# Performance work log

Hardware: AMD Instinct MI355X
Metric: run time of the kernel (lower is better)

Reference implementation:

```python
import jax, jax.numpy as jnp
import numpy as np

HIDDEN = 2048
NUM_Q_HEADS = 32
NUM_KV_HEADS = 8
HEAD_DIM = HIDDEN // NUM_Q_HEADS  # 64
GROUPS = NUM_Q_HEADS // NUM_KV_HEADS  # 4
MAX_WAVELENGTH = 10000.0
B, S = 2, 1024
NEG_INF = -1e9  # keras Softmax masking constant


def apply_rope(x, start_index=0, max_wavelength=MAX_WAVELENGTH):
    # x: [b, s, h, d]; keras_hub RotaryEmbedding (split-half / Llama style)
    d = x.shape[-1]
    s = x.shape[1]
    freq_range = jnp.arange(0, d, 2, dtype=jnp.float32)
    inverse_freq = 1.0 / (max_wavelength ** (freq_range / d))  # [d/2]
    positions = jnp.arange(s, dtype=jnp.float32) + start_index
    freq = positions[:, None] * inverse_freq[None, :]  # [s, d/2]
    emb = jnp.concatenate([freq, freq], axis=-1)[None, :, None, :]  # [1,s,1,d]
    cos = jnp.cos(emb).astype(x.dtype)
    sin = jnp.sin(emb).astype(x.dtype)
    x1, x2 = jnp.split(x, 2, axis=-1)
    half_rot = jnp.concatenate([-x2, x1], axis=-1)
    return x * cos + half_rot * sin


def setup_inputs() -> dict:
    key = jax.random.key(0)
    k1, k2, k3, k4, k5 = jax.random.split(key, 5)
    hidden_states = jax.random.normal(k1, (B, S, HIDDEN), dtype=jnp.float32)
    # causal mask, broadcast over batch
    attention_mask = jnp.broadcast_to(
        jnp.tril(jnp.ones((S, S), dtype=bool))[None], (B, S, S)
    )
    scale = 1.0 / np.sqrt(HIDDEN)
    Wq = jax.random.normal(k2, (HIDDEN, NUM_Q_HEADS * HEAD_DIM), dtype=jnp.float32) * scale
    Wk = jax.random.normal(k3, (HIDDEN, NUM_KV_HEADS * HEAD_DIM), dtype=jnp.float32) * scale
    Wv = jax.random.normal(k4, (HIDDEN, NUM_KV_HEADS * HEAD_DIM), dtype=jnp.float32) * scale
    Wo = jax.random.normal(k5, (NUM_Q_HEADS * HEAD_DIM, HIDDEN), dtype=jnp.float32) * scale
    return {"hidden_states": hidden_states, "attention_mask": attention_mask,
            "Wq": Wq, "Wk": Wk, "Wv": Wv, "Wo": Wo}


def reference(hidden_states, attention_mask, Wq, Wk, Wv, Wo):
    b, s, _ = hidden_states.shape
    q = (hidden_states @ Wq).reshape(b, s, NUM_Q_HEADS, HEAD_DIM)
    k = (hidden_states @ Wk).reshape(b, s, NUM_KV_HEADS, HEAD_DIM)
    v = (hidden_states @ Wv).reshape(b, s, NUM_KV_HEADS, HEAD_DIM)
    q = apply_rope(q)
    k = apply_rope(k)
    # GQA: repeat kv heads to match query heads (ops.repeat on axis 2)
    k = jnp.repeat(k, GROUPS, axis=2)
    v = jnp.repeat(v, GROUPS, axis=2)
    inv_norm = 1.0 / np.sqrt(HEAD_DIM)
    scores = jnp.einsum("bquh,bkuh->buqk", q, k) * inv_norm  # [b, h, q, k]
    scores = scores.astype(jnp.float32)
    scores = jnp.where(attention_mask[:, None, :, :], scores, NEG_INF)
    probs = jax.nn.softmax(scores, axis=-1).astype(hidden_states.dtype)
    attn = jnp.einsum("buqk,bkuh->bquh", probs, v)  # [b, q, h, hd]
    attn = attn.reshape(b, s, HIDDEN)
    return attn @ Wo
```

## Files before the change

### kernel.cpp

```cpp
#include <hip/hip_runtime.h>
#include <hip/hip_bf16.h>
#include <math.h>

#define S_LEN 1024
#define BATCH 2
#define HIDDEN 2048
#define NQH 32
#define NKVH 8
#define HD 64
#define LDQKV 3072
#define M_ROWS (BATCH * S_LEN)

typedef __attribute__((ext_vector_type(8))) short bf16x8;
typedef __attribute__((ext_vector_type(4))) float f32x4;

typedef unsigned int uint32_g __attribute__((address_space(1)));
typedef unsigned int uint32_l __attribute__((address_space(3)));

static __device__ __forceinline__ void load_lds16(const void* g, void* l) {
    __builtin_amdgcn_global_load_lds((const uint32_g*)g, (uint32_l*)l, 16, 0, 0);
}

static __device__ __forceinline__ short f2bf(float f) {
    union { __hip_bfloat16 h; short s; } cv;
    cv.h = __float2bfloat16(f);
    return cv.s;
}

__global__ __launch_bounds__(256) void conv_all_kernel(
    const float* __restrict__ X,
    const float* __restrict__ Wq, const float* __restrict__ Wk,
    const float* __restrict__ Wv, const float* __restrict__ Wo,
    short* __restrict__ Xb, short* __restrict__ Wqkvt, short* __restrict__ Wot,
    float2* __restrict__ cs2)
{
    __shared__ short Ts[64][68];
    const int tid = threadIdx.x;

    if (blockIdx.z == 4) {
        int flat = blockIdx.y * 32 + blockIdx.x;
        size_t base = (size_t)flat * 4096 + (size_t)tid * 16;
        #pragma unroll
        for (int rep = 0; rep < 2; ++rep) {
            size_t i = base + rep * 8;
            float4 a = *reinterpret_cast<const float4*>(X + i);
            float4 b = *reinterpret_cast<const float4*>(X + i + 4);
            union { bf16x8 v; short s[8]; } t;
            t.s[0] = f2bf(a.x); t.s[1] = f2bf(a.y); t.s[2] = f2bf(a.z); t.s[3] = f2bf(a.w);
            t.s[4] = f2bf(b.x); t.s[5] = f2bf(b.y); t.s[6] = f2bf(b.z); t.s[7] = f2bf(b.w);
            *reinterpret_cast<bf16x8*>(Xb + i) = t.v;
        }
        if (flat < 128) {
            int g = flat * 256 + tid;
            int s = g >> 5, i = g & 31;
            float inv_freq = 1.0f / powf(10000.0f, (float)i / 32.0f);
            float freq = (float)s * inv_freq;
            double sn, cs;
            sincos((double)freq, &sn, &cs);
            cs2[g] = make_float2((float)cs, (float)sn);
        }
        return;
    }

    const float* src; short* dst; int N;
    switch (blockIdx.z) {
        case 0: src = Wq; dst = Wqkvt;                         N = 2048; break;
        case 1: src = Wk; dst = Wqkvt + (size_t)2048 * 2048;   N = 512;  break;
        case 2: src = Wv; dst = Wqkvt + (size_t)2560 * 2048;   N = 512;  break;
        default: src = Wo; dst = Wot;                          N = 2048; break;
    }
    const int n0 = blockIdx.x * 64, k0 = blockIdx.y * 64;
    if (n0 >= N) return;

    #pragma unroll
    for (int rep = 0; rep < 4; ++rep) {
        int idx = rep * 256 + tid;
        int row = idx >> 4, c4 = (idx & 15) * 4;
        float4 v = *reinterpret_cast<const float4*>(
            src + (size_t)(k0 + row) * N + n0 + c4);
        ushort4 u;
        u.x = (unsigned short)f2bf(v.x); u.y = (unsigned short)f2bf(v.y);
        u.z = (unsigned short)f2bf(v.z); u.w = (unsigned short)f2bf(v.w);
        *reinterpret_cast<ushort4*>(&Ts[row][c4]) = u;
    }
    __syncthreads();
    #pragma unroll
    for (int rep = 0; rep < 2; ++rep) {
        int idx = rep * 256 + tid;
        int n = idx >> 3, kc = (idx & 7) * 8;
        union { bf16x8 v; short s[8]; } t;
        #pragma unroll
        for (int j = 0; j < 8; ++j) t.s[j] = Ts[kc + j][n];
        *reinterpret_cast<bf16x8*>(dst + (size_t)(n0 + n) * 2048 + k0 + kc) = t.v;
    }
}

template <bool ROPE_BF16>
__global__ __launch_bounds__(256) void gemm_bf16_kernel(
    const short* __restrict__ A, const short* __restrict__ Bt,
    float* __restrict__ C, short* __restrict__ Cb,
    short* __restrict__ vt_g,
    const float2* __restrict__ cs2, int K, int ldc)
{
    const int n0 = blockIdx.x * 64, m0 = blockIdx.y * 128;
    const int tid = threadIdx.x;
    const int w = tid >> 6, lane = tid & 63;
    const int m15 = lane & 15, q4 = lane >> 4;

    __shared__ short SL[2][128 * 64 + 64 * 64];

    f32x4 acc[2][4];
    #pragma unroll
    for (int i = 0; i < 2; ++i)
        #pragma unroll
        for (int j = 0; j < 4; ++j) acc[i][j] = (f32x4){0.f, 0.f, 0.f, 0.f};

    const int srow = lane >> 3;
    const int pchunk = lane & 7;

#define GSTAGE(bf_, k0_) do {                                                 \
    short (*As_)[64] = (short(*)[64])SL[bf_];                                 \
    short (*Bs_)[64] = (short(*)[64])(SL[bf_] + 128 * 64);                    \
    _Pragma("unroll")                                                         \
    for (int r = 0; r < 4; ++r) {                                             \
        int row = (w * 4 + r) * 8 + srow;                         \
        int lchunk = pchunk ^ (row & 7);                                      \
        load_lds16(A + (size_t)(m0 + row) * K + (k0_) + lchunk * 8,           \
                   &As_[(w * 4 + r) * 8][0]);                                 \
    }                                                                         \
    _Pragma("unroll")                                                         \
    for (int r = 0; r < 2; ++r) {                                             \
        int row = (w * 2 + r) * 8 + srow;                          \
        int lchunk = pchunk ^ (row & 7);                                      \
        load_lds16(Bt + (size_t)(n0 + row) * K + (k0_) + lchunk * 8,          \
                   &Bs_[(w * 2 + r) * 8][0]);                                 \
    }                                                                         \
} while (0)

    GSTAGE(0, 0);
    __syncthreads();

    const int nkt = K >> 6;
    for (int kt = 0; kt < nkt; ++kt) {
        const int bf = kt & 1;
        if (kt + 1 < nkt) GSTAGE(bf ^ 1, (kt + 1) * 64);

        short (*As)[64] = (short(*)[64])SL[bf];
        short (*Bs)[64] = (short(*)[64])(SL[bf] + 128 * 64);
        #pragma unroll
        for (int ch = 0; ch < 2; ++ch) {
            bf16x8 af[2], bff[4];
            #pragma unroll
            for (int mt = 0; mt < 2; ++mt) {
                int row = w * 32 + mt * 16 + m15;
                af[mt] = *reinterpret_cast<const bf16x8*>(
                    &As[row][(((ch * 4 + q4) ^ (row & 7))) * 8]);
            }
            #pragma unroll
            for (int nt = 0; nt < 4; ++nt) {
                int row = nt * 16 + m15;
                bff[nt] = *reinterpret_cast<const bf16x8*>(
                    &Bs[row][(((ch * 4 + q4) ^ (row & 7))) * 8]);
            }
            #pragma unroll
            for (int mt = 0; mt < 2; ++mt)
                #pragma unroll
                for (int nt = 0; nt < 4; ++nt)
                    acc[mt][nt] = __builtin_amdgcn_mfma_f32_16x16x32_bf16(
                        af[mt], bff[nt], acc[mt][nt], 0, 0, 0);
        }
        __syncthreads();
    }
#undef GSTAGE

    if (!ROPE_BF16) {
        #pragma unroll
        for (int mt = 0; mt < 2; ++mt)
            #pragma unroll
            for (int nt = 0; nt < 4; ++nt)
                #pragma unroll
                for (int reg = 0; reg < 4; ++reg)
                    C[(size_t)(m0 + w * 32 + mt * 16 + q4 * 4 + reg) * ldc
                      + n0 + nt * 16 + m15] = acc[mt][nt][reg];
    } else if (n0 < 2560) {
        #pragma unroll
        for (int mt = 0; mt < 2; ++mt) {
            #pragma unroll
            for (int reg = 0; reg < 4; ++reg) {
                int row = m0 + w * 32 + mt * 16 + q4 * 4 + reg;
                int s = row & (S_LEN - 1);
                float2 t0 = cs2[s * 32 + m15];
                float2 t1 = cs2[s * 32 + 16 + m15];
                float a0 = acc[mt][0][reg], a1 = acc[mt][1][reg];
                float a2 = acc[mt][2][reg], a3 = acc[mt][3][reg];
                size_t base = (size_t)row * ldc + n0 + m15;
                Cb[base +  0] = f2bf(a0 * t0.x - a2 * t0.y);
                Cb[base + 16] = f2bf(a1 * t1.x - a3 * t1.y);
                Cb[base + 32] = f2bf(a2 * t0.x + a0 * t0.y);
                Cb[base + 48] = f2bf(a3 * t1.x + a1 * t1.y);
            }
        }
    } else {
        __syncthreads();
        short (*VT)[136] = (short(*)[136])SL[0];
        #pragma unroll
        for (int mt = 0; mt < 2; ++mt) {
            #pragma unroll
            for (int nt = 0; nt < 4; ++nt) {
                ushort4 u;
                u.x = (unsigned short)f2bf(acc[mt][nt][0]);
                u.y = (unsigned short)f2bf(acc[mt][nt][1]);
                u.z = (unsigned short)f2bf(acc[mt][nt][2]);
                u.w = (unsigned short)f2bf(acc[mt][nt][3]);
                *reinterpret_cast<ushort4*>(
                    &VT[nt * 16 + m15][w * 32 + mt * 16 + q4 * 4]) = u;
            }
        }
        __syncthreads();
        const int kvh = (n0 - 2560) >> 6;
        const int b = m0 >> 10, k0loc = m0 & (S_LEN - 1);
        const int dim = tid >> 2, kc = (tid & 3) * 32;
        short* dst = vt_g + (size_t)((b * 8 + kvh) * 64 + dim) * S_LEN + k0loc + kc;
        #pragma unroll
        for (int u = 0; u < 4; ++u)
            *reinterpret_cast<bf16x8*>(dst + u * 8) =
                *reinterpret_cast<const bf16x8*>(&VT[dim][kc + u * 8]);
    }
}

__global__ __launch_bounds__(512, 4) void attn_kernel(
    const short* __restrict__ qkvb, const short* __restrict__ vt_g,
    short* __restrict__ attn_b)
{
    const int i  = blockIdx.x;
    const int h  = blockIdx.y;
    const int b  = blockIdx.z;
    const int qtA = i;
    const int qtB = 15 - i;
    const int tid = threadIdx.x;
    const int w = tid >> 6, lane = tid & 63;
    const int kvh = h >> 2;
    const int m15 = lane & 15, q4 = lane >> 4;

    __shared__ short Ks[2][64][64];
    __shared__ short Vt[2][64][64];

    const int qt_w = (w < 4) ? qtB : qtA;
    const int rowbase = qt_w * 64 + (w & 3) * 16;

    const bf16x8 qf0 = *reinterpret_cast<const bf16x8*>(
        qkvb + (size_t)(b * S_LEN + rowbase + m15) * LDQKV + h * HD + q4 * 8);
    const bf16x8 qf1 = *reinterpret_cast<const bf16x8*>(
        qkvb + (size_t)(b * S_LEN + rowbase + m15) * LDQKV + h * HD + 32 + q4 * 8);

    f32x4 o4[4];
    #pragma unroll
    for (int k = 0; k < 4; ++k) o4[k] = (f32x4){0.f, 0.f, 0.f, 0.f};
    float lsum = 0.f;

    const int r8 = lane >> 3, p8 = lane & 7;
    const int lch = (p8 ^ r8) * 8;
    const short* kbase = qkvb + (size_t)(b * S_LEN) * LDQKV + 2048 + kvh * HD;
    const short* vbase = vt_g + (size_t)(b * 8 + kvh) * 64 * S_LEN;

#define STAGE(bf_, t) do {                                                    \
    int row_ = w * 8 + r8;                                                    \
    load_lds16(kbase + (size_t)((t) * 64 + row_) * LDQKV + lch,               \
               &Ks[bf_][w * 8][0]);                                           \
    load_lds16(vbase + (size_t)row_ * S_LEN + (t) * 64 + lch,                 \
               &Vt[bf_][w * 8][0]);                                           \
} while (0)

#define COMPUTE(bf_, t) do {                                                  \
    const int xr_ = m15 & 7;                                                  \
    float p_[4][4];                                                           \
    _Pragma("unroll")                                                         \
    for (int nt = 0; nt < 4; ++nt) {                                          \
        f32x4 acc = (f32x4){0.f, 0.f, 0.f, 0.f};                              \
        bf16x8 kf0 = *reinterpret_cast<const bf16x8*>(                        \
            &Ks[bf_][nt * 16 + m15][(q4 ^ xr_) * 8]);                         \
        bf16x8 kf1 = *reinterpret_cast<const bf16x8*>(                        \
            &Ks[bf_][nt * 16 + m15][((4 + q4) ^ xr_) * 8]);                   \
        acc = __builtin_amdgcn_mfma_f32_16x16x32_bf16(kf0, qf0, acc, 0, 0, 0);\
        acc = __builtin_amdgcn_mfma_f32_16x16x32_bf16(kf1, qf1, acc, 0, 0, 0);\
        _Pragma("unroll")                                                     \
        for (int reg = 0; reg < 4; ++reg)                                     \
            p_[nt][reg] = exp2f(fminf(acc[reg] * 0.180336880f, 80.f));        \
    }                                                                         \
    if ((t) * 64 + 63 > rowbase) {            \
        const int rowg_ = rowbase + m15;                                      \
        _Pragma("unroll")                                                     \
        for (int nt = 0; nt < 4; ++nt)                                        \
            _Pragma("unroll")                                                 \
            for (int reg = 0; reg < 4; ++reg)                                 \
                if ((t) * 64 + nt * 16 + q4 * 4 + reg > rowg_)                \
                    p_[nt][reg] = 0.f;                                        \
    }                                                                         \
    _Pragma("unroll")                                                         \
    for (int nt = 0; nt < 4; ++nt)                                            \
        _Pragma("unroll")                                                     \
        for (int reg = 0; reg < 4; ++reg) lsum += p_[nt][reg];                \
    unsigned lo_[4], hi_[4];                                                  \
    _Pragma("unroll")                                                         \
    for (int nt = 0; nt < 4; ++nt) {                                          \
        lo_[nt] = (unsigned)(unsigned short)f2bf(p_[nt][0])                   \
                | ((unsigned)(unsigned short)f2bf(p_[nt][1]) << 16);          \
        hi_[nt] = (unsigned)(unsigned short)f2bf(p_[nt][2])                   \
                | ((unsigned)(unsigned short)f2bf(p_[nt][3]) << 16);          \
    }                                                                         \
    const int La_ = ((q4 & 1) * 2) * 16 + m15;                                \
    const int Lb_ = La_ + 16;                                                 \
    const int hiH_ = q4 >> 1;                                                 \
    bf16x8 pf_[2];                                                            \
    _Pragma("unroll")                                                         \
    for (int ch = 0; ch < 2; ++ch) {                                          \
        int a0 = __shfl((int)lo_[ch * 2],     La_, 64);                       \
        int a1 = __shfl((int)hi_[ch * 2],     La_, 64);                       \
        int a2 = __shfl((int)lo_[ch * 2],     Lb_, 64);                       \
        int a3 = __shfl((int)hi_[ch * 2],     Lb_, 64);                       \
        int b0 = __shfl((int)lo_[ch * 2 + 1], La_, 64);                       \
        int b1 = __shfl((int)hi_[ch * 2 + 1], La_, 64);                       \
        int b2 = __shfl((int)lo_[ch * 2 + 1], Lb_, 64);                       \
        int b3 = __shfl((int)hi_[ch * 2 + 1], Lb_, 64);                       \
        union { int ii[4]; bf16x8 v; } u_;                                    \
        u_.ii[0] = hiH_ ? b0 : a0;                                            \
        u_.ii[1] = hiH_ ? b1 : a1;                                            \
        u_.ii[2] = hiH_ ? b2 : a2;                                            \
        u_.ii[3] = hiH_ ? b3 : a3;                                            \
        pf_[ch] = u_.v;                                                       \
    }                                                                         \
    _Pragma("unroll")                                                         \
    for (int nt2 = 0; nt2 < 4; ++nt2) {                                       \
        bf16x8 vf0 = *reinterpret_cast<const bf16x8*>(                        \
            &Vt[bf_][nt2 * 16 + m15][(q4 ^ xr_) * 8]);                        \
        bf16x8 vf1 = *reinterpret_cast<const bf16x8*>(                        \
            &Vt[bf_][nt2 * 16 + m15][((4 + q4) ^ xr_) * 8]);                  \
        o4[nt2] = __builtin_amdgcn_mfma_f32_16x16x32_bf16(                    \
            pf_[0], vf0, o4[nt2], 0, 0, 0);                                   \
        o4[nt2] = __builtin_amdgcn_mfma_f32_16x16x32_bf16(                    \
            pf_[1], vf1, o4[nt2], 0, 0, 0);                                   \
    }                                                                         \
} while (0)

    STAGE(0, 0);
    __syncthreads();

    for (int t = 0; t <= qtB; ++t) {
        const int bf = t & 1;
        if (t < qtB) STAGE(bf ^ 1, t + 1);
        if (t <= qt_w) COMPUTE(bf, t);
        __syncthreads();
    }

#undef STAGE
#undef COMPUTE

    float l = lsum;
    l += __shfl_xor(l, 16, 64);
    l += __shfl_xor(l, 32, 64);
    float invl = 1.0f / l;
    float invl4[4];
    #pragma unroll
    for (int reg = 0; reg < 4; ++reg)
        invl4[reg] = __shfl(invl, q4 * 4 + reg, 64);

    #pragma unroll
    for (int nt2 = 0; nt2 < 4; ++nt2)
        #pragma unroll
        for (int reg = 0; reg < 4; ++reg)
            attn_b[(size_t)(b * S_LEN + rowbase + q4 * 4 + reg) * HIDDEN
                   + h * HD + nt2 * 16 + m15] = f2bf(o4[nt2][reg] * invl4[reg]);
}

extern "C" void kernel_launch(void* const* d_in, const int* in_sizes, int n_in,
                              void* d_out, int out_size, void* d_ws, size_t ws_size,
                              hipStream_t stream) {
    const float* X  = (const float*)d_in[0];
    const float* Wq = (const float*)d_in[2];
    const float* Wk = (const float*)d_in[3];
    const float* Wv = (const float*)d_in[4];
    const float* Wo = (const float*)d_in[5];
    float* out = (float*)d_out;

    short*  qkvb  = (short*)d_ws;
    short*  Xb    = qkvb + (size_t)M_ROWS * LDQKV;
    short*  Wqkvt = Xb + (size_t)HIDDEN * HIDDEN;
    short*  Wot   = Wqkvt + (size_t)LDQKV * HIDDEN;
    short*  vt_g  = Wot + (size_t)HIDDEN * HIDDEN;
    float2* cs2   = (float2*)(vt_g + (size_t)16 * 64 * S_LEN);
    short*  attn_b = Xb;

    conv_all_kernel<<<dim3(32, 32, 5), dim3(256), 0, stream>>>(
        X, Wq, Wk, Wv, Wo, Xb, Wqkvt, Wot, cs2);

    gemm_bf16_kernel<true><<<dim3(48, 16), dim3(256), 0, stream>>>(
        Xb, Wqkvt, nullptr, qkvb, vt_g, cs2, 2048, LDQKV);
    attn_kernel<<<dim3(8, 32, 2), dim3(512), 0, stream>>>(qkvb, vt_g, attn_b);
    gemm_bf16_kernel<false><<<dim3(32, 16), dim3(256), 0, stream>>>(
        attn_b, Wot, out, nullptr, nullptr, nullptr, 2048, HIDDEN);
}
```

Measured before the change: 194.7 us.

## Load K and V fragments directly from global memory, dropping LDS staging

Removes the double-buffered LDS staging of K and V tiles, along with the per-tile block-wide barriers, in the attention kernel. Each wave now reads its K and V MFMA fragments straight from global memory (relying on L1/L2 caching) and loops only up to its own causal tile count. This removes the synchronisation and LDS traffic, and lets each wave run independently of the others. The cost is that the eight waves fetch the same K/V data redundantly from cache, and the global loads have higher latency with no prefetch overlap.

```diff
diff --git a/kernel.cpp b/kernel.cpp
--- a/kernel.cpp
+++ b/kernel.cpp
@@ -242,9 +242,6 @@
     const int kvh = h >> 2;
     const int m15 = lane & 15, q4 = lane >> 4;
 
-    __shared__ short Ks[2][64][64];
-    __shared__ short Vt[2][64][64];
-
     const int qt_w = (w < 4) ? qtB : qtA;
     const int rowbase = qt_w * 64 + (w & 3) * 16;
 
@@ -258,29 +255,18 @@
     for (int k = 0; k < 4; ++k) o4[k] = (f32x4){0.f, 0.f, 0.f, 0.f};
     float lsum = 0.f;
 
-    const int r8 = lane >> 3, p8 = lane & 7;
-    const int lch = (p8 ^ r8) * 8;
     const short* kbase = qkvb + (size_t)(b * S_LEN) * LDQKV + 2048 + kvh * HD;
     const short* vbase = vt_g + (size_t)(b * 8 + kvh) * 64 * S_LEN;
 
-#define STAGE(bf_, t) do {                                                    \
-    int row_ = w * 8 + r8;                                                    \
-    load_lds16(kbase + (size_t)((t) * 64 + row_) * LDQKV + lch,               \
-               &Ks[bf_][w * 8][0]);                                           \
-    load_lds16(vbase + (size_t)row_ * S_LEN + (t) * 64 + lch,                 \
-               &Vt[bf_][w * 8][0]);                                           \
-} while (0)
-
-#define COMPUTE(bf_, t) do {                                                  \
-    const int xr_ = m15 & 7;                                                  \
+#define COMPUTE(t) do {                                                       \
     float p_[4][4];                                                           \
     _Pragma("unroll")                                                         \
     for (int nt = 0; nt < 4; ++nt) {                                          \
         f32x4 acc = (f32x4){0.f, 0.f, 0.f, 0.f};                              \
-        bf16x8 kf0 = *reinterpret_cast<const bf16x8*>(                        \
-            &Ks[bf_][nt * 16 + m15][(q4 ^ xr_) * 8]);                         \
-        bf16x8 kf1 = *reinterpret_cast<const bf16x8*>(                        \
-            &Ks[bf_][nt * 16 + m15][((4 + q4) ^ xr_) * 8]);                   \
+        const short* krow_ = kbase                                            \
+            + (size_t)((t) * 64 + nt * 16 + m15) * LDQKV;                     \
+        bf16x8 kf0 = *reinterpret_cast<const bf16x8*>(krow_ + q4 * 8);        \
+        bf16x8 kf1 = *reinterpret_cast<const bf16x8*>(krow_ + 32 + q4 * 8);   \
         acc = __builtin_amdgcn_mfma_f32_16x16x32_bf16(kf0, qf0, acc, 0, 0, 0);\
         acc = __builtin_amdgcn_mfma_f32_16x16x32_bf16(kf1, qf1, acc, 0, 0, 0);\
         _Pragma("unroll")                                                     \
@@ -331,10 +317,10 @@
     }                                                                         \
     _Pragma("unroll")                                                         \
     for (int nt2 = 0; nt2 < 4; ++nt2) {                                       \
-        bf16x8 vf0 = *reinterpret_cast<const bf16x8*>(                        \
-            &Vt[bf_][nt2 * 16 + m15][(q4 ^ xr_) * 8]);                        \
-        bf16x8 vf1 = *reinterpret_cast<const bf16x8*>(                        \
-            &Vt[bf_][nt2 * 16 + m15][((4 + q4) ^ xr_) * 8]);                  \
+        const short* vrow_ = vbase                                            \
+            + (size_t)(nt2 * 16 + m15) * S_LEN + (t) * 64;                    \
+        bf16x8 vf0 = *reinterpret_cast<const bf16x8*>(vrow_ + q4 * 8);        \
+        bf16x8 vf1 = *reinterpret_cast<const bf16x8*>(vrow_ + 32 + q4 * 8);   \
         o4[nt2] = __builtin_amdgcn_mfma_f32_16x16x32_bf16(                    \
             pf_[0], vf0, o4[nt2], 0, 0, 0);                                   \
         o4[nt2] = __builtin_amdgcn_mfma_f32_16x16x32_bf16(                    \
@@ -342,17 +328,10 @@
     }                                                                         \
 } while (0)
 
-    STAGE(0, 0);
-    __syncthreads();
-
-    for (int t = 0; t <= qtB; ++t) {
-        const int bf = t & 1;
-        if (t < qtB) STAGE(bf ^ 1, t + 1);
-        if (t <= qt_w) COMPUTE(bf, t);
-        __syncthreads();
-    }
-
-#undef STAGE
+    for (int t = 0; t <= qt_w; ++t) {
+        COMPUTE(t);
+    }
+
 #undef COMPUTE
 
     float l = lsum;
```

After: 232.4 us. +19.4%, slower.

## Balance causal attention waves by splitting long query tile KV range across idle waves

Applied to the files above, without the earlier changes.

The attention kernel pairs query tiles i and 15-i per block. Previously the waves on the short tile sat idle while the waves on the long tile walked up to 16 KV tiles. Now the loop runs 9 iterations. Once the short tile is finished, its waves process the later KV tiles of the long tile into separate accumulators, and the partial outputs and row sums are merged through LDS at the end. This shortens the critical path per block. In exchange it doubles the LDS buffers, stages two KV tiles per iteration, and adds a merge step with an extra barrier.

```diff
diff --git a/kernel.cpp b/kernel.cpp
--- a/kernel.cpp
+++ b/kernel.cpp
@@ -241,54 +241,62 @@
     const int w = tid >> 6, lane = tid & 63;
     const int kvh = h >> 2;
     const int m15 = lane & 15, q4 = lane >> 4;
-
-    __shared__ short Ks[2][64][64];
-    __shared__ short Vt[2][64][64];
-
-    const int qt_w = (w < 4) ? qtB : qtA;
-    const int rowbase = qt_w * 64 + (w & 3) * 16;
-
-    const bf16x8 qf0 = *reinterpret_cast<const bf16x8*>(
-        qkvb + (size_t)(b * S_LEN + rowbase + m15) * LDQKV + h * HD + q4 * 8);
-    const bf16x8 qf1 = *reinterpret_cast<const bf16x8*>(
-        qkvb + (size_t)(b * S_LEN + rowbase + m15) * LDQKV + h * HD + 32 + q4 * 8);
-
-    f32x4 o4[4];
+    const int wq = w & 3;
+
+    __shared__ short Ks[2][2][64][64];
+    __shared__ short Vt[2][2][64][64];
+
+    const int rowbaseB = qtB * 64 + wq * 16;
+    const int rowbaseA = qtA * 64 + wq * 16;
+
+    const bf16x8 qfB0 = *reinterpret_cast<const bf16x8*>(
+        qkvb + (size_t)(b * S_LEN + rowbaseB + m15) * LDQKV + h * HD + q4 * 8);
+    const bf16x8 qfB1 = *reinterpret_cast<const bf16x8*>(
+        qkvb + (size_t)(b * S_LEN + rowbaseB + m15) * LDQKV + h * HD + 32 + q4 * 8);
+    const bf16x8 qfA0 = *reinterpret_cast<const bf16x8*>(
+        qkvb + (size_t)(b * S_LEN + rowbaseA + m15) * LDQKV + h * HD + q4 * 8);
+    const bf16x8 qfA1 = *reinterpret_cast<const bf16x8*>(
+        qkvb + (size_t)(b * S_LEN + rowbaseA + m15) * LDQKV + h * HD + 32 + q4 * 8);
+
+    f32x4 oB[4], oA[4];
     #pragma unroll
-    for (int k = 0; k < 4; ++k) o4[k] = (f32x4){0.f, 0.f, 0.f, 0.f};
-    float lsum = 0.f;
+    for (int k = 0; k < 4; ++k) {
+        oB[k] = (f32x4){0.f, 0.f, 0.f, 0.f};
+        oA[k] = (f32x4){0.f, 0.f, 0.f, 0.f};
+    }
+    float lB = 0.f, lA = 0.f;
 
     const int r8 = lane >> 3, p8 = lane & 7;
     const int lch = (p8 ^ r8) * 8;
     const short* kbase = qkvb + (size_t)(b * S_LEN) * LDQKV + 2048 + kvh * HD;
     const short* vbase = vt_g + (size_t)(b * 8 + kvh) * 64 * S_LEN;
 
-#define STAGE(bf_, t) do {                                                    \
+#define STAGE(bf_, sl_, tk) do {                                              \
     int row_ = w * 8 + r8;                                                    \
-    load_lds16(kbase + (size_t)((t) * 64 + row_) * LDQKV + lch,               \
-               &Ks[bf_][w * 8][0]);                                           \
-    load_lds16(vbase + (size_t)row_ * S_LEN + (t) * 64 + lch,                 \
-               &Vt[bf_][w * 8][0]);                                           \
+    load_lds16(kbase + (size_t)((tk) * 64 + row_) * LDQKV + lch,              \
+               &Ks[bf_][sl_][w * 8][0]);                                      \
+    load_lds16(vbase + (size_t)row_ * S_LEN + (tk) * 64 + lch,                \
+               &Vt[bf_][sl_][w * 8][0]);                                      \
 } while (0)
 
-#define COMPUTE(bf_, t) do {                                                  \
+#define COMPUTE(bf_, sl_, t, rb_, o_, ls_, qa_, qb_) do {                     \
     const int xr_ = m15 & 7;                                                  \
     float p_[4][4];                                                           \
     _Pragma("unroll")                                                         \
     for (int nt = 0; nt < 4; ++nt) {                                          \
         f32x4 acc = (f32x4){0.f, 0.f, 0.f, 0.f};                              \
         bf16x8 kf0 = *reinterpret_cast<const bf16x8*>(                        \
-            &Ks[bf_][nt * 16 + m15][(q4 ^ xr_) * 8]);                         \
+            &Ks[bf_][sl_][nt * 16 + m15][(q4 ^ xr_) * 8]);                    \
         bf16x8 kf1 = *reinterpret_cast<const bf16x8*>(                        \
-            &Ks[bf_][nt * 16 + m15][((4 + q4) ^ xr_) * 8]);                   \
-        acc = __builtin_amdgcn_mfma_f32_16x16x32_bf16(kf0, qf0, acc, 0, 0, 0);\
-        acc = __builtin_amdgcn_mfma_f32_16x16x32_bf16(kf1, qf1, acc, 0, 0, 0);\
+            &Ks[bf_][sl_][nt * 16 + m15][((4 + q4) ^ xr_) * 8]);              \
+        acc = __builtin_amdgcn_mfma_f32_16x16x32_bf16(kf0, qa_, acc, 0, 0, 0);\
+        acc = __builtin_amdgcn_mfma_f32_16x16x32_bf16(kf1, qb_, acc, 0, 0, 0);\
         _Pragma("unroll")                                                     \
         for (int reg = 0; reg < 4; ++reg)                                     \
             p_[nt][reg] = exp2f(fminf(acc[reg] * 0.180336880f, 80.f));        \
     }                                                                         \
-    if ((t) * 64 + 63 > rowbase) {            \
-        const int rowg_ = rowbase + m15;                                      \
+    if ((t) * 64 + 63 > (rb_)) {              \
+        const int rowg_ = (rb_) + m15;                                        \
         _Pragma("unroll")                                                     \
         for (int nt = 0; nt < 4; ++nt)                                        \
             _Pragma("unroll")                                                 \
@@ -299,7 +307,7 @@
     _Pragma("unroll")                                                         \
     for (int nt = 0; nt < 4; ++nt)                                            \
         _Pragma("unroll")                                                     \
-        for (int reg = 0; reg < 4; ++reg) lsum += p_[nt][reg];                \
+        for (int reg = 0; reg < 4; ++reg) (ls_) += p_[nt][reg];               \
     unsigned lo_[4], hi_[4];                                                  \
     _Pragma("unroll")                                                         \
     for (int nt = 0; nt < 4; ++nt) {                                          \
@@ -332,44 +340,93 @@
     _Pragma("unroll")                                                         \
     for (int nt2 = 0; nt2 < 4; ++nt2) {                                       \
         bf16x8 vf0 = *reinterpret_cast<const bf16x8*>(                        \
-            &Vt[bf_][nt2 * 16 + m15][(q4 ^ xr_) * 8]);                        \
+            &Vt[bf_][sl_][nt2 * 16 + m15][(q4 ^ xr_) * 8]);                   \
         bf16x8 vf1 = *reinterpret_cast<const bf16x8*>(                        \
-            &Vt[bf_][nt2 * 16 + m15][((4 + q4) ^ xr_) * 8]);                  \
-        o4[nt2] = __builtin_amdgcn_mfma_f32_16x16x32_bf16(                    \
-            pf_[0], vf0, o4[nt2], 0, 0, 0);                                   \
-        o4[nt2] = __builtin_amdgcn_mfma_f32_16x16x32_bf16(                    \
-            pf_[1], vf1, o4[nt2], 0, 0, 0);                                   \
+            &Vt[bf_][sl_][nt2 * 16 + m15][((4 + q4) ^ xr_) * 8]);             \
+        (o_)[nt2] = __builtin_amdgcn_mfma_f32_16x16x32_bf16(                  \
+            pf_[0], vf0, (o_)[nt2], 0, 0, 0);                                 \
+        (o_)[nt2] = __builtin_amdgcn_mfma_f32_16x16x32_bf16(                  \
+            pf_[1], vf1, (o_)[nt2], 0, 0, 0);                                 \
     }                                                                         \
 } while (0)
 
-    STAGE(0, 0);
+    STAGE(0, 0, 0);
     __syncthreads();
 
-    for (int t = 0; t <= qtB; ++t) {
-        const int bf = t & 1;
-        if (t < qtB) STAGE(bf ^ 1, t + 1);
-        if (t <= qt_w) COMPUTE(bf, t);
+    for (int it = 0; it <= 8; ++it) {
+        const int bf = it & 1;
+        const int next = it + 1;
+        if (next <= 8) STAGE(bf ^ 1, 0, next);
+        if (next <= 7 && next > i) STAGE(bf ^ 1, 1, 8 + next - i);
+        if (w < 4) {
+            COMPUTE(bf, 0, it, rowbaseB, oB, lB, qfB0, qfB1);
+        } else if (it <= 7) {
+            if (it <= i) {
+                COMPUTE(bf, 0, it, rowbaseA, oA, lA, qfA0, qfA1);
+            } else {
+                const int tkv = 8 + it - i;
+                COMPUTE(bf, 1, tkv, rowbaseB, oB, lB, qfB0, qfB1);
+            }
+        }
         __syncthreads();
     }
 
 #undef STAGE
 #undef COMPUTE
 
-    float l = lsum;
+    float l = lB;
     l += __shfl_xor(l, 16, 64);
     l += __shfl_xor(l, 32, 64);
-    float invl = 1.0f / l;
-    float invl4[4];
-    #pragma unroll
-    for (int reg = 0; reg < 4; ++reg)
-        invl4[reg] = __shfl(invl, q4 * 4 + reg, 64);
-
-    #pragma unroll
-    for (int nt2 = 0; nt2 < 4; ++nt2)
+
+    float* MB = (float*)&Ks[0][0][0][0];
+    if (w >= 4) {
+        float* dst = MB + ((size_t)(wq * 64 + lane)) * 17;
+        #pragma unroll
+        for (int nt2 = 0; nt2 < 4; ++nt2)
+            #pragma unroll
+            for (int reg = 0; reg < 4; ++reg)
+                dst[nt2 * 4 + reg] = oB[nt2][reg];
+        dst[16] = l;
+    }
+    __syncthreads();
+
+    if (w < 4) {
+        const float* src = MB + ((size_t)(wq * 64 + lane)) * 17;
+        #pragma unroll
+        for (int nt2 = 0; nt2 < 4; ++nt2)
+            #pragma unroll
+            for (int reg = 0; reg < 4; ++reg)
+                oB[nt2][reg] += src[nt2 * 4 + reg];
+        l += src[16];
+        float invl = 1.0f / l;
+        float invl4[4];
         #pragma unroll
         for (int reg = 0; reg < 4; ++reg)
-            attn_b[(size_t)(b * S_LEN + rowbase + q4 * 4 + reg) * HIDDEN
-                   + h * HD + nt2 * 16 + m15] = f2bf(o4[nt2][reg] * invl4[reg]);
+            invl4[reg] = __shfl(invl, q4 * 4 + reg, 64);
+        #pragma unroll
+        for (int nt2 = 0; nt2 < 4; ++nt2)
+            #pragma unroll
+            for (int reg = 0; reg < 4; ++reg)
+                attn_b[(size_t)(b * S_LEN + rowbaseB + q4 * 4 + reg) * HIDDEN
+                       + h * HD + nt2 * 16 + m15] =
+                    f2bf(oB[nt2][reg] * invl4[reg]);
+    } else {
+        float la = lA;
+        la += __shfl_xor(la, 16, 64);
+        la += __shfl_xor(la, 32, 64);
+        float invl = 1.0f / la;
+        float invl4[4];
+        #pragma unroll
+        for (int reg = 0; reg < 4; ++reg)
+            invl4[reg] = __shfl(invl, q4 * 4 + reg, 64);
+        #pragma unroll
+        for (int nt2 = 0; nt2 < 4; ++nt2)
+            #pragma unroll
+            for (int reg = 0; reg < 4; ++reg)
+                attn_b[(size_t)(b * S_LEN + rowbaseA + q4 * 4 + reg) * HIDDEN
+                       + h * HD + nt2 * 16 + m15] =
+                    f2bf(oA[nt2][reg] * invl4[reg]);
+    }
 }
 
 extern "C" void kernel_launch(void* const* d_in, const int* in_sizes, int n_in,
```

Result: no change. 194.1 us (-0.3%).
